# Kernel optimization log

Hardware: AMD Instinct MI355X
Metric: run time of the kernel (lower is better)

## Reference

```python
import jax, jax.numpy as jnp
import numpy as np

EPS = 1e-06


def setup_inputs() -> dict:
    key = jax.random.key(0)
    k1, k2, k3 = jax.random.split(key, 3)
    B, L, S, C = 128, 512, 512, 64
    q = jax.random.normal(k1, (B, L, C), dtype=jnp.float32)
    k = jax.random.normal(k2, (B, S, C), dtype=jnp.float32)
    labels = jax.random.randint(k3, (B, L, S), 0, 2, dtype=jnp.int64)
    return {"q": q, "k": k, "labels": labels}


def reference(q, k, labels):
    # sim: [B, L, S], mapped to (0, 1) via (1 + cos-like sim) / 2
    sim = (1.0 + jnp.einsum('blc,bsc->bls', q, k)) * 0.5

    # column-wise stats (over L) -> [B, S]; torch.std uses ddof=1 (unbiased)
    col = (jnp.max(sim, axis=1) - jnp.mean(sim, axis=1)) / jnp.std(sim, axis=1, ddof=1)
    sharp1 = jax.nn.softmax(col, axis=-1)  # [B, S]

    # row-wise stats (over S) -> [B, L]
    row = (jnp.max(sim, axis=2) - jnp.mean(sim, axis=2)) / jnp.std(sim, axis=2, ddof=1)
    sharp2 = jax.nn.softmax(row, axis=-1)  # [B, L]

    simc = jnp.clip(sim, EPS, 1.0 - EPS)
    nll = -jnp.log(simc)                    # [B, L, S]
    nll_neg = -jnp.log(1.0 - simc)          # [B, L, S]

    pos = (labels == 1).astype(sim.dtype)
    neg = (labels == 0).astype(sim.dtype)

    # masked sums per sample, weighted by sharpness (broadcast over rows/cols)
    loss1 = jnp.sum(nll * sharp1[:, None, :] * pos, axis=(1, 2))  # [B]
    loss2 = jnp.sum(nll * sharp2[:, :, None] * pos, axis=(1, 2))  # [B]
    loss3 = jnp.sum(nll_neg * neg, axis=(1, 2)) / jnp.sum(neg, axis=(1, 2))  # [B]

    losses = (loss1 + loss2) * 0.5 + loss3
    return (sharp1, jnp.mean(losses))
```

## Files before the change

kernel.cpp:

```cpp
#include <hip/hip_runtime.h>

#define EPSF 1e-6f

constexpr int B = 128, L = 512, S = 512, C = 64;
constexpr int TILE_R = 64;
constexpr int TILES  = L / TILE_R;
constexpr int CHUNK  = 64;
constexpr int NCHUNK = S / CHUNK;
constexpr int STR    = 68;

constexpr size_t WS_COLMAX = 0;
constexpr size_t WS_COLSUM = WS_COLMAX + (size_t)B * TILES * S;
constexpr size_t WS_COLSSQ = WS_COLSUM + (size_t)B * TILES * S;
constexpr size_t WS_COLP1  = WS_COLSSQ + (size_t)B * TILES * S;
constexpr size_t WS_ROWMAX = WS_COLP1  + (size_t)B * TILES * S;
constexpr size_t WS_ROWSUM = WS_ROWMAX + (size_t)B * L;
constexpr size_t WS_ROWSSQ = WS_ROWSUM + (size_t)B * L;
constexpr size_t WS_ROWP2  = WS_ROWSSQ + (size_t)B * L;
constexpr size_t WS_NEGS   = WS_ROWP2  + (size_t)B * L;
constexpr size_t WS_NEGC   = WS_NEGS   + (size_t)B * TILES;

__device__ inline void stage_T(const float* __restrict__ g, float (*lds)[STR], int tid)
{
    const int r0 = (tid & 15) * 4;
    const int c0 = (tid >> 4) * 4;
    float4 r0v = *(const float4*)&g[(r0 + 0) * 64 + c0];
    float4 r1v = *(const float4*)&g[(r0 + 1) * 64 + c0];
    float4 r2v = *(const float4*)&g[(r0 + 2) * 64 + c0];
    float4 r3v = *(const float4*)&g[(r0 + 3) * 64 + c0];
    *(float4*)&lds[c0 + 0][r0] = make_float4(r0v.x, r1v.x, r2v.x, r3v.x);
    *(float4*)&lds[c0 + 1][r0] = make_float4(r0v.y, r1v.y, r2v.y, r3v.y);
    *(float4*)&lds[c0 + 2][r0] = make_float4(r0v.z, r1v.z, r2v.z, r3v.z);
    *(float4*)&lds[c0 + 3][r0] = make_float4(r0v.w, r1v.w, r2v.w, r3v.w);
}

__global__ __launch_bounds__(256, 4)
void pass1_kernel(const float* __restrict__ q, const float* __restrict__ kmat,
                  const int* __restrict__ labels, float* __restrict__ ws)
{
    __shared__ float qs[C][STR];
    __shared__ float ks[C][STR];
    __shared__ float colred[4][CHUNK][4];
    __shared__ float nred[4][2];

    const int bidx = blockIdx.x;
    const int b    = bidx / TILES;
    const int tile = bidx % TILES;
    const int tid  = threadIdx.x;
    const int tx   = tid & 15;
    const int ty   = tid >> 4;
    const int lane = tid & 63;
    const int wave = tid >> 6;
    const int rowbase = tile * TILE_R;
    const int r0 = ty * 4;
    const int c0 = tx * 4;

    float* colmax_p = ws + WS_COLMAX;
    float* colsum_p = ws + WS_COLSUM;
    float* colssq_p = ws + WS_COLSSQ;
    float* colp1_p  = ws + WS_COLP1;
    float* rowmax_p = ws + WS_ROWMAX;
    float* rowsum_p = ws + WS_ROWSUM;
    float* rowssq_p = ws + WS_ROWSSQ;
    float* rowp2_p  = ws + WS_ROWP2;
    float* negs_p   = ws + WS_NEGS;
    float* negc_p   = ws + WS_NEGC;

    stage_T(q + ((size_t)b * L + rowbase) * C, qs, tid);

    float rmax[4], rsum[4], rssq[4], rp2[4];
#pragma unroll
    for (int i = 0; i < 4; ++i) { rmax[i] = -3.4e38f; rsum[i] = 0.f; rssq[i] = 0.f; rp2[i] = 0.f; }
    float negsum = 0.f, negcnt = 0.f;

    const float* kb = kmat + (size_t)b * S * C;
    const int*   lb = labels + ((size_t)b * L + rowbase) * S;

    for (int ch = 0; ch < NCHUNK; ++ch) {
        __syncthreads();
        stage_T(kb + (size_t)ch * CHUNK * C, ks, tid);
        __syncthreads();

        float acc[4][4];
#pragma unroll
        for (int i = 0; i < 4; ++i)
#pragma unroll
            for (int j = 0; j < 4; ++j) acc[i][j] = 0.f;

#pragma unroll 4
        for (int kk = 0; kk < C; ++kk) {
            float4 av = *(const float4*)&qs[kk][r0];
            float4 bv = *(const float4*)&ks[kk][c0];
            float a[4] = {av.x, av.y, av.z, av.w};
            float bb[4] = {bv.x, bv.y, bv.z, bv.w};
#pragma unroll
            for (int i = 0; i < 4; ++i)
#pragma unroll
                for (int j = 0; j < 4; ++j)
                    acc[i][j] = fmaf(a[i], bb[j], acc[i][j]);
        }

        float cmax[4], csum[4], cssq[4], cp1[4];
#pragma unroll
        for (int j = 0; j < 4; ++j) { cmax[j] = -3.4e38f; csum[j] = 0.f; cssq[j] = 0.f; cp1[j] = 0.f; }

#pragma unroll
        for (int i = 0; i < 4; ++i) {
            const int* lrow = lb + (size_t)(r0 + i) * S + ch * CHUNK + c0;
            int4 lv = *(const int4*)lrow;
            int labv[4] = {lv.x, lv.y, lv.z, lv.w};
#pragma unroll
            for (int j = 0; j < 4; ++j) {
                float sim = fmaf(0.5f, acc[i][j], 0.5f);
                rmax[i] = fmaxf(rmax[i], sim);
                rsum[i] += sim;
                rssq[i] = fmaf(sim, sim, rssq[i]);
                cmax[j] = fmaxf(cmax[j], sim);
                csum[j] += sim;
                cssq[j] = fmaf(sim, sim, cssq[j]);
                float sc  = fminf(fmaxf(sim, EPSF), 1.f - EPSF);
                bool  isp = (labv[j] == 1);
                float pos = isp ? 1.f : 0.f;
                float t   = isp ? sc : (1.f - sc);
                float nl  = -__logf(t);
                float pn  = pos * nl;
                rp2[i] += pn;
                cp1[j] += pn;
                negsum += nl - pn;
                negcnt += 1.f - pos;
            }
        }

#pragma unroll
        for (int j = 0; j < 4; ++j) {
#pragma unroll
            for (int m = 16; m <= 32; m <<= 1) {
                cmax[j] = fmaxf(cmax[j], __shfl_xor(cmax[j], m, 64));
                csum[j] += __shfl_xor(csum[j], m, 64);
                cssq[j] += __shfl_xor(cssq[j], m, 64);
                cp1[j]  += __shfl_xor(cp1[j],  m, 64);
            }
        }
        if (lane < 16) {
#pragma unroll
            for (int j = 0; j < 4; ++j) {
                colred[wave][lane * 4 + j][0] = cmax[j];
                colred[wave][lane * 4 + j][1] = csum[j];
                colred[wave][lane * 4 + j][2] = cssq[j];
                colred[wave][lane * 4 + j][3] = cp1[j];
            }
        }
        __syncthreads();
        if (tid < CHUNK) {
            float m0 = colred[0][tid][0], s1 = colred[0][tid][1];
            float s2 = colred[0][tid][2], pp = colred[0][tid][3];
#pragma unroll
            for (int w = 1; w < 4; ++w) {
                m0 = fmaxf(m0, colred[w][tid][0]);
                s1 += colred[w][tid][1];
                s2 += colred[w][tid][2];
                pp += colred[w][tid][3];
            }
            size_t idx = ((size_t)b * TILES + tile) * S + ch * CHUNK + tid;
            colmax_p[idx] = m0; colsum_p[idx] = s1; colssq_p[idx] = s2; colp1_p[idx] = pp;
        }
    }

#pragma unroll
    for (int i = 0; i < 4; ++i) {
#pragma unroll
        for (int m = 1; m <= 8; m <<= 1) {
            rmax[i] = fmaxf(rmax[i], __shfl_xor(rmax[i], m, 64));
            rsum[i] += __shfl_xor(rsum[i], m, 64);
            rssq[i] += __shfl_xor(rssq[i], m, 64);
            rp2[i]  += __shfl_xor(rp2[i],  m, 64);
        }
    }
    if (tx == 0) {
#pragma unroll
        for (int i = 0; i < 4; ++i) {
            size_t idx = (size_t)b * L + rowbase + r0 + i;
            rowmax_p[idx] = rmax[i]; rowsum_p[idx] = rsum[i];
            rowssq_p[idx] = rssq[i]; rowp2_p[idx]  = rp2[i];
        }
    }

#pragma unroll
    for (int m = 1; m <= 32; m <<= 1) {
        negsum += __shfl_xor(negsum, m, 64);
        negcnt += __shfl_xor(negcnt, m, 64);
    }
    if (lane == 0) { nred[wave][0] = negsum; nred[wave][1] = negcnt; }
    __syncthreads();
    if (tid == 0) {
        float ns = 0.f, nc = 0.f;
        for (int w = 0; w < 4; ++w) { ns += nred[w][0]; nc += nred[w][1]; }
        negs_p[bidx] = ns; negc_p[bidx] = nc;
    }
}

template <bool MAX>
__device__ inline float bred(float v, float* red)
{
#pragma unroll
    for (int m = 1; m <= 32; m <<= 1) {
        float o = __shfl_xor(v, m, 64);
        v = MAX ? fmaxf(v, o) : (v + o);
    }
    const int wave = threadIdx.x >> 6;
    const int lane = threadIdx.x & 63;
    if (lane == 0) red[wave] = v;
    __syncthreads();
    if (threadIdx.x == 0) {
        float r = red[0];
        for (int w = 1; w < 8; ++w) r = MAX ? fmaxf(r, red[w]) : (r + red[w]);
        red[8] = r;
    }
    __syncthreads();
    float out = red[8];
    __syncthreads();
    return out;
}

__global__ __launch_bounds__(512)
void pass2_kernel(const float* __restrict__ ws, float* __restrict__ out)
{
    __shared__ float red[9];
    const int b = blockIdx.x;
    const int s = threadIdx.x;

    if (blockIdx.y == 0) {
        const float* colmax_p = ws + WS_COLMAX;
        const float* colsum_p = ws + WS_COLSUM;
        const float* colssq_p = ws + WS_COLSSQ;
        const float* colp1_p  = ws + WS_COLP1;

        float m = -3.4e38f, sm = 0.f, sq = 0.f, p1 = 0.f;
#pragma unroll
        for (int t = 0; t < TILES; ++t) {
            size_t idx = ((size_t)b * TILES + t) * S + s;
            m = fmaxf(m, colmax_p[idx]);
            sm += colsum_p[idx];
            sq += colssq_p[idx];
            p1 += colp1_p[idx];
        }
        float mean  = sm * (1.f / L);
        float var   = (sq - sm * sm * (1.f / L)) * (1.f / (L - 1));
        float score = (m - mean) / sqrtf(var);

        float gmax = bred<true>(score, red);
        float e    = __expf(score - gmax);
        float esum = bred<false>(e, red);
        float sharp1 = e / esum;
        out[(size_t)b * S + s] = sharp1;
        float loss1 = bred<false>(sharp1 * p1, red);
        if (s == 0) atomicAdd(out + (size_t)B * S, loss1 * (0.5f / B));
    } else {
        const float* rowmax_p = ws + WS_ROWMAX;
        const float* rowsum_p = ws + WS_ROWSUM;
        const float* rowssq_p = ws + WS_ROWSSQ;
        const float* rowp2_p  = ws + WS_ROWP2;
        const float* negs_p   = ws + WS_NEGS;
        const float* negc_p   = ws + WS_NEGC;

        size_t ridx = (size_t)b * L + s;
        float m2 = rowmax_p[ridx], sm2 = rowsum_p[ridx];
        float sq2 = rowssq_p[ridx], p2 = rowp2_p[ridx];
        float mean2  = sm2 * (1.f / S);
        float var2   = (sq2 - sm2 * sm2 * (1.f / S)) * (1.f / (S - 1));
        float score2 = (m2 - mean2) / sqrtf(var2);

        float gmax2 = bred<true>(score2, red);
        float e2    = __expf(score2 - gmax2);
        float esum2 = bred<false>(e2, red);
        float loss2 = bred<false>((e2 / esum2) * p2, red);

        if (s == 0) {
            float ns = 0.f, nc = 0.f;
            for (int t = 0; t < TILES; ++t) { ns += negs_p[b * TILES + t]; nc += negc_p[b * TILES + t]; }
            atomicAdd(out + (size_t)B * S, (0.5f * loss2 + ns / nc) * (1.f / B));
        }
    }
}

extern "C" void kernel_launch(void* const* d_in, const int* in_sizes, int n_in,
                              void* d_out, int out_size, void* d_ws, size_t ws_size,
                              hipStream_t stream)
{
    const float* q      = (const float*)d_in[0];
    const float* k      = (const float*)d_in[1];
    const int*   labels = (const int*)d_in[2];
    float* out = (float*)d_out;
    float* ws  = (float*)d_ws;

    hipMemsetAsync((char*)d_out + (size_t)B * S * sizeof(float), 0, sizeof(float), stream);

    pass1_kernel<<<dim3(B * TILES), dim3(256), 0, stream>>>(q, k, labels, ws);
    pass2_kernel<<<dim3(B, 2), dim3(512), 0, stream>>>(ws, out);
}
```

Baseline: 282.1 us.

## Compute similarity tile with split-fp16 MFMA instead of scalar FP32 FMAs

Replaces the scalar FP32 outer-product GEMM in pass1 with MFMA 16x16x32 f16 instructions. Each fp32 operand is split into hi and lo halves, and three products (hh, hl, lh) are summed to approximate fp32 accuracy. The staging and LDS layouts are rewritten to match MFMA fragment ordering, and the epilogue is remapped to the MFMA output layout. Label loads become scalar per-element reads instead of int4 vectors, which may hurt coalescing. The split-fp16 scheme adds small precision error.

```diff
diff --git a/kernel.cpp b/kernel.cpp
--- a/kernel.cpp
+++ b/kernel.cpp
@@ -1,13 +1,15 @@
 #include <hip/hip_runtime.h>
 
 #define EPSF 1e-6f
+
+typedef _Float16 half8 __attribute__((ext_vector_type(8)));
+typedef float f32x4 __attribute__((ext_vector_type(4)));
 
 constexpr int B = 128, L = 512, S = 512, C = 64;
 constexpr int TILE_R = 64;
 constexpr int TILES  = L / TILE_R;
 constexpr int CHUNK  = 64;
 constexpr int NCHUNK = S / CHUNK;
-constexpr int STR    = 68;
 
 constexpr size_t WS_COLMAX = 0;
 constexpr size_t WS_COLSUM = WS_COLMAX + (size_t)B * TILES * S;
@@ -20,40 +22,54 @@
 constexpr size_t WS_NEGS   = WS_ROWP2  + (size_t)B * L;
 constexpr size_t WS_NEGC   = WS_NEGS   + (size_t)B * TILES;
 
-__device__ inline void stage_T(const float* __restrict__ g, float (*lds)[STR], int tid)
-{
-    const int r0 = (tid & 15) * 4;
-    const int c0 = (tid >> 4) * 4;
-    float4 r0v = *(const float4*)&g[(r0 + 0) * 64 + c0];
-    float4 r1v = *(const float4*)&g[(r0 + 1) * 64 + c0];
-    float4 r2v = *(const float4*)&g[(r0 + 2) * 64 + c0];
-    float4 r3v = *(const float4*)&g[(r0 + 3) * 64 + c0];
-    *(float4*)&lds[c0 + 0][r0] = make_float4(r0v.x, r1v.x, r2v.x, r3v.x);
-    *(float4*)&lds[c0 + 1][r0] = make_float4(r0v.y, r1v.y, r2v.y, r3v.y);
-    *(float4*)&lds[c0 + 2][r0] = make_float4(r0v.z, r1v.z, r2v.z, r3v.z);
-    *(float4*)&lds[c0 + 3][r0] = make_float4(r0v.w, r1v.w, r2v.w, r3v.w);
+__device__ inline void stageF(const float* __restrict__ g,
+                              half8 (*__restrict__ hiA)[64],
+                              half8 (*__restrict__ loA)[64], int t)
+{
+    const int row = t >> 2, c0 = (t & 3) * 16;
+    const float* src = g + row * 64 + c0;
+    float4 v0 = *(const float4*)(src);
+    float4 v1 = *(const float4*)(src + 4);
+    float4 v2 = *(const float4*)(src + 8);
+    float4 v3 = *(const float4*)(src + 12);
+    float v[16] = {v0.x, v0.y, v0.z, v0.w, v1.x, v1.y, v1.z, v1.w,
+                   v2.x, v2.y, v2.z, v2.w, v3.x, v3.y, v3.z, v3.w};
+#pragma unroll
+    for (int o = 0; o < 2; ++o) {
+        const int cb   = c0 + o * 8;
+        const int idx  = (row >> 4) * 2 + (cb >> 5);
+        const int lane_s = (((cb >> 3) & 3) << 4) + (row & 15);
+        half8 h, l;
+#pragma unroll
+        for (int j = 0; j < 8; ++j) {
+            float f = v[o * 8 + j];
+            _Float16 hi = (_Float16)f;
+            h[j] = hi;
+            l[j] = (_Float16)(f - (float)hi);
+        }
+        hiA[idx][lane_s] = h;
+        loA[idx][lane_s] = l;
+    }
 }
 
 __global__ __launch_bounds__(256, 4)
 void pass1_kernel(const float* __restrict__ q, const float* __restrict__ kmat,
                   const int* __restrict__ labels, float* __restrict__ ws)
 {
-    __shared__ float qs[C][STR];
-    __shared__ float ks[C][STR];
-    __shared__ float colred[4][CHUNK][4];
+    __shared__ half8 qhiF[8][64], qloF[8][64];
+    __shared__ half8 khiF[8][64], kloF[8][64];
+    __shared__ float4 colred4[4][CHUNK];
     __shared__ float nred[4][2];
 
     const int bidx = blockIdx.x;
     const int b    = bidx / TILES;
     const int tile = bidx % TILES;
     const int tid  = threadIdx.x;
-    const int tx   = tid & 15;
-    const int ty   = tid >> 4;
     const int lane = tid & 63;
     const int wave = tid >> 6;
+    const int l15  = lane & 15;
+    const int quad = lane >> 4;
     const int rowbase = tile * TILE_R;
-    const int r0 = ty * 4;
-    const int c0 = tx * 4;
 
     float* colmax_p = ws + WS_COLMAX;
     float* colsum_p = ws + WS_COLSUM;
@@ -66,7 +82,7 @@
     float* negs_p   = ws + WS_NEGS;
     float* negc_p   = ws + WS_NEGC;
 
-    stage_T(q + ((size_t)b * L + rowbase) * C, qs, tid);
+    stageF(q + ((size_t)b * L + rowbase) * C, qhiF, qloF, tid);
 
     float rmax[4], rsum[4], rssq[4], rp2[4];
 #pragma unroll
@@ -78,88 +94,81 @@
 
     for (int ch = 0; ch < NCHUNK; ++ch) {
         __syncthreads();
-        stage_T(kb + (size_t)ch * CHUNK * C, ks, tid);
+        stageF(kb + (size_t)ch * CHUNK * C, khiF, kloF, tid);
         __syncthreads();
 
-        float acc[4][4];
-#pragma unroll
-        for (int i = 0; i < 4; ++i)
-#pragma unroll
-            for (int j = 0; j < 4; ++j) acc[i][j] = 0.f;
-
-#pragma unroll 4
-        for (int kk = 0; kk < C; ++kk) {
-            float4 av = *(const float4*)&qs[kk][r0];
-            float4 bv = *(const float4*)&ks[kk][c0];
-            float a[4] = {av.x, av.y, av.z, av.w};
-            float bb[4] = {bv.x, bv.y, bv.z, bv.w};
-#pragma unroll
-            for (int i = 0; i < 4; ++i)
-#pragma unroll
-                for (int j = 0; j < 4; ++j)
-                    acc[i][j] = fmaf(a[i], bb[j], acc[i][j]);
+        half8 ah0 = qhiF[wave * 2 + 0][lane], ah1 = qhiF[wave * 2 + 1][lane];
+        half8 al0 = qloF[wave * 2 + 0][lane], al1 = qloF[wave * 2 + 1][lane];
+
+        f32x4 acc[4];
+#pragma unroll
+        for (int ct = 0; ct < 4; ++ct) {
+            half8 bh0 = khiF[ct * 2 + 0][lane], bh1 = khiF[ct * 2 + 1][lane];
+            half8 bl0 = kloF[ct * 2 + 0][lane], bl1 = kloF[ct * 2 + 1][lane];
+            f32x4 a = {0.f, 0.f, 0.f, 0.f};
+            a = __builtin_amdgcn_mfma_f32_16x16x32_f16(ah0, bh0, a, 0, 0, 0);
+            a = __builtin_amdgcn_mfma_f32_16x16x32_f16(ah0, bl0, a, 0, 0, 0);
+            a = __builtin_amdgcn_mfma_f32_16x16x32_f16(al0, bh0, a, 0, 0, 0);
+            a = __builtin_amdgcn_mfma_f32_16x16x32_f16(ah1, bh1, a, 0, 0, 0);
+            a = __builtin_amdgcn_mfma_f32_16x16x32_f16(ah1, bl1, a, 0, 0, 0);
+            a = __builtin_amdgcn_mfma_f32_16x16x32_f16(al1, bh1, a, 0, 0, 0);
+            acc[ct] = a;
         }
 
         float cmax[4], csum[4], cssq[4], cp1[4];
 #pragma unroll
-        for (int j = 0; j < 4; ++j) { cmax[j] = -3.4e38f; csum[j] = 0.f; cssq[j] = 0.f; cp1[j] = 0.f; }
-
-#pragma unroll
-        for (int i = 0; i < 4; ++i) {
-            const int* lrow = lb + (size_t)(r0 + i) * S + ch * CHUNK + c0;
-            int4 lv = *(const int4*)lrow;
-            int labv[4] = {lv.x, lv.y, lv.z, lv.w};
-#pragma unroll
-            for (int j = 0; j < 4; ++j) {
-                float sim = fmaf(0.5f, acc[i][j], 0.5f);
-                rmax[i] = fmaxf(rmax[i], sim);
-                rsum[i] += sim;
-                rssq[i] = fmaf(sim, sim, rssq[i]);
-                cmax[j] = fmaxf(cmax[j], sim);
-                csum[j] += sim;
-                cssq[j] = fmaf(sim, sim, cssq[j]);
+        for (int ct = 0; ct < 4; ++ct) { cmax[ct] = -3.4e38f; csum[ct] = 0.f; cssq[ct] = 0.f; cp1[ct] = 0.f; }
+
+#pragma unroll
+        for (int ct = 0; ct < 4; ++ct) {
+            const int colg = ch * CHUNK + ct * 16 + l15;
+#pragma unroll
+            for (int r = 0; r < 4; ++r) {
+                const int rowl = wave * 16 + quad * 4 + r;
+                int lab = lb[(size_t)rowl * S + colg];
+                float sim = fmaf(0.5f, acc[ct][r], 0.5f);
+                rmax[r] = fmaxf(rmax[r], sim);
+                rsum[r] += sim;
+                rssq[r] = fmaf(sim, sim, rssq[r]);
+                cmax[ct] = fmaxf(cmax[ct], sim);
+                csum[ct] += sim;
+                cssq[ct] = fmaf(sim, sim, cssq[ct]);
                 float sc  = fminf(fmaxf(sim, EPSF), 1.f - EPSF);
-                bool  isp = (labv[j] == 1);
+                bool  isp = (lab == 1);
                 float pos = isp ? 1.f : 0.f;
                 float t   = isp ? sc : (1.f - sc);
                 float nl  = -__logf(t);
                 float pn  = pos * nl;
-                rp2[i] += pn;
-                cp1[j] += pn;
+                rp2[r] += pn;
+                cp1[ct] += pn;
                 negsum += nl - pn;
                 negcnt += 1.f - pos;
             }
         }
 
 #pragma unroll
-        for (int j = 0; j < 4; ++j) {
+        for (int ct = 0; ct < 4; ++ct) {
 #pragma unroll
             for (int m = 16; m <= 32; m <<= 1) {
-                cmax[j] = fmaxf(cmax[j], __shfl_xor(cmax[j], m, 64));
-                csum[j] += __shfl_xor(csum[j], m, 64);
-                cssq[j] += __shfl_xor(cssq[j], m, 64);
-                cp1[j]  += __shfl_xor(cp1[j],  m, 64);
+                cmax[ct] = fmaxf(cmax[ct], __shfl_xor(cmax[ct], m, 64));
+                csum[ct] += __shfl_xor(csum[ct], m, 64);
+                cssq[ct] += __shfl_xor(cssq[ct], m, 64);
+                cp1[ct]  += __shfl_xor(cp1[ct],  m, 64);
             }
         }
         if (lane < 16) {
 #pragma unroll
-            for (int j = 0; j < 4; ++j) {
-                colred[wave][lane * 4 + j][0] = cmax[j];
-                colred[wave][lane * 4 + j][1] = csum[j];
-                colred[wave][lane * 4 + j][2] = cssq[j];
-                colred[wave][lane * 4 + j][3] = cp1[j];
-            }
+            for (int ct = 0; ct < 4; ++ct)
+                colred4[wave][ct * 16 + l15] = make_float4(cmax[ct], csum[ct], cssq[ct], cp1[ct]);
         }
         __syncthreads();
         if (tid < CHUNK) {
-            float m0 = colred[0][tid][0], s1 = colred[0][tid][1];
-            float s2 = colred[0][tid][2], pp = colred[0][tid][3];
+            float4 v = colred4[0][tid];
+            float m0 = v.x, s1 = v.y, s2 = v.z, pp = v.w;
 #pragma unroll
             for (int w = 1; w < 4; ++w) {
-                m0 = fmaxf(m0, colred[w][tid][0]);
-                s1 += colred[w][tid][1];
-                s2 += colred[w][tid][2];
-                pp += colred[w][tid][3];
+                float4 u = colred4[w][tid];
+                m0 = fmaxf(m0, u.x); s1 += u.y; s2 += u.z; pp += u.w;
             }
             size_t idx = ((size_t)b * TILES + tile) * S + ch * CHUNK + tid;
             colmax_p[idx] = m0; colsum_p[idx] = s1; colssq_p[idx] = s2; colp1_p[idx] = pp;
@@ -167,21 +176,21 @@
     }
 
 #pragma unroll
-    for (int i = 0; i < 4; ++i) {
+    for (int r = 0; r < 4; ++r) {
 #pragma unroll
         for (int m = 1; m <= 8; m <<= 1) {
-            rmax[i] = fmaxf(rmax[i], __shfl_xor(rmax[i], m, 64));
-            rsum[i] += __shfl_xor(rsum[i], m, 64);
-            rssq[i] += __shfl_xor(rssq[i], m, 64);
-            rp2[i]  += __shfl_xor(rp2[i],  m, 64);
-        }
-    }
-    if (tx == 0) {
-#pragma unroll
-        for (int i = 0; i < 4; ++i) {
-            size_t idx = (size_t)b * L + rowbase + r0 + i;
-            rowmax_p[idx] = rmax[i]; rowsum_p[idx] = rsum[i];
-            rowssq_p[idx] = rssq[i]; rowp2_p[idx]  = rp2[i];
+            rmax[r] = fmaxf(rmax[r], __shfl_xor(rmax[r], m, 64));
+            rsum[r] += __shfl_xor(rsum[r], m, 64);
+            rssq[r] += __shfl_xor(rssq[r], m, 64);
+            rp2[r]  += __shfl_xor(rp2[r],  m, 64);
+        }
+    }
+    if (l15 == 0) {
+#pragma unroll
+        for (int r = 0; r < 4; ++r) {
+            size_t idx = (size_t)b * L + rowbase + wave * 16 + quad * 4 + r;
+            rowmax_p[idx] = rmax[r]; rowsum_p[idx] = rsum[r];
+            rowssq_p[idx] = rssq[r]; rowp2_p[idx]  = rp2[r];
         }
     }
 
```

New measurement: 274.5 us. 1.03x faster.
